# Kernel optimization log

Hardware: AMD Instinct MI355X
Metric: run time of the kernel (lower is better)

## Reference

```python
import jax, jax.numpy as jnp
import numpy as np

B, Q, D = 16, 1000, 256
HH, LV, NP = 8, 4, 4          # heads, levels, points per level
DH = D // HH                  # head dim = 32
TP = LV * NP                  # total points = 16
SHAPES = np.array([[64, 64], [32, 32], [16, 16], [8, 8]], dtype=np.int64)
LTOT = int((SHAPES[:, 0] * SHAPES[:, 1]).sum())  # 5440


def setup_inputs() -> dict:
    key = jax.random.key(0)
    ks = jax.random.split(key, 10)
    query = jax.random.normal(ks[0], (B, Q, D), dtype=jnp.float32)
    reference_points = jax.random.uniform(ks[1], (B, Q, LV, 2), dtype=jnp.float32)
    input_flatten = jax.random.normal(ks[2], (B, LTOT, D), dtype=jnp.float32)
    start = np.concatenate([[0], np.cumsum(SHAPES[:, 0] * SHAPES[:, 1])[:-1]])

    # params (mimic reset_parameters: directional bias init for offsets)
    thetas = np.arange(HH, dtype=np.float32) * (2.0 * np.pi / HH)
    grid = np.stack([np.cos(thetas), np.sin(thetas)], -1)
    grid = grid / np.abs(grid).max(-1, keepdims=True)
    grid = np.tile(grid[:, None, :], (1, TP, 1))  # [HH, TP, 2]
    scaling = np.concatenate([np.arange(1, NP + 1, dtype=np.float32) for _ in range(LV)]).reshape(1, TP, 1)
    bo = jnp.asarray((grid * scaling).reshape(-1), dtype=jnp.float32)

    s = 1.0 / np.sqrt(D)
    Wv = jax.random.normal(ks[3], (D, D), dtype=jnp.float32) * s
    bv = jnp.zeros((D,), dtype=jnp.float32)
    Wo = jax.random.normal(ks[4], (D, HH * TP * 2), dtype=jnp.float32) * 0.005
    Wa = jax.random.normal(ks[5], (D, HH * TP), dtype=jnp.float32) * 0.02
    ba = jnp.zeros((HH * TP,), dtype=jnp.float32)
    Wout = jax.random.normal(ks[6], (D, D), dtype=jnp.float32) * s
    bout = jnp.zeros((D,), dtype=jnp.float32)

    return {
        "query": query, "reference_points": reference_points, "input_flatten": input_flatten,
        "input_spatial_shapes": jnp.asarray(SHAPES), "input_level_start_index": jnp.asarray(start),
        "Wv": Wv, "bv": bv, "Wo": Wo, "bo": bo, "Wa": Wa, "ba": ba, "Wout": Wout, "bout": bout,
    }


def _sample_bilinear(val_flat, loc, Hl, Wl):
    # val_flat: [B, HH, DH, Hl*Wl]; loc: [B, Q, HH, p, 2] normalized in [0,1]
    # grid_sample align_corners=False, zeros padding: pixel = loc*size - 0.5
    b, q, h, p, _ = loc.shape
    x = loc[..., 0] * Wl - 0.5
    y = loc[..., 1] * Hl - 0.5
    x0 = jnp.floor(x); y0 = jnp.floor(y)
    lx = x - x0; ly = y - y0
    x0i = x0.astype(jnp.int32); y0i = y0.astype(jnp.int32)
    acc = jnp.zeros((b, h, val_flat.shape[2], q, p), dtype=val_flat.dtype)
    for ix, iy, w in ((x0i, y0i, (1 - lx) * (1 - ly)),
                      (x0i + 1, y0i, lx * (1 - ly)),
                      (x0i, y0i + 1, (1 - lx) * ly),
                      (x0i + 1, y0i + 1, lx * ly)):
        valid = ((ix >= 0) & (ix < Wl) & (iy >= 0) & (iy < Hl)).astype(val_flat.dtype)
        idx = jnp.clip(iy, 0, Hl - 1) * Wl + jnp.clip(ix, 0, Wl - 1)   # [B,Q,HH,p]
        idx = idx.transpose(0, 2, 1, 3).reshape(b, h, 1, q * p)
        v = jnp.take_along_axis(val_flat, idx, axis=3).reshape(b, h, -1, q, p)
        acc = acc + v * ((w * valid).transpose(0, 2, 1, 3)[:, :, None])
    return acc  # [B, HH, DH, Q, p]


def reference(query, reference_points, input_flatten, input_spatial_shapes,
              input_level_start_index, Wv, bv, Wo, bo, Wa, ba, Wout, bout):
    shapes = np.asarray(input_spatial_shapes)  # static level shapes
    shapes = shapes if shapes.any() else SHAPES  # fallback if zeros placeholder
    b, q, d = query.shape

    value = (input_flatten @ Wv + bv).reshape(b, -1, HH, DH)          # [B,L,HH,DH]
    off = (query @ Wo + bo).reshape(b, q, HH, LV, NP, 2)              # offsets
    attn = jax.nn.softmax((query @ Wa + ba).reshape(b, q, HH, TP), axis=-1)
    attn = attn.reshape(b, q, HH, LV, NP)

    # normalizer [LV,2] = (W_l, H_l)
    norm = jnp.stack([jnp.asarray(shapes[:, 1]), jnp.asarray(shapes[:, 0])], -1).astype(query.dtype)
    loc = reference_points[:, :, None, :, None, :] + off / norm[None, None, None, :, None, :]
    # loc: [B,Q,HH,LV,NP,2]

    out = jnp.zeros((b, HH, DH, q), dtype=query.dtype)
    start = 0
    for lvl in range(LV):
        Hl, Wl = int(shapes[lvl, 0]), int(shapes[lvl, 1])
        n = Hl * Wl
        val_l = value[:, start:start + n].transpose(0, 2, 3, 1)       # [B,HH,DH,n]
        start += n
        samp = _sample_bilinear(val_l, loc[:, :, :, lvl], Hl, Wl)     # [B,HH,DH,Q,NP]
        aw = attn[:, :, :, lvl].transpose(0, 2, 1, 3)                 # [B,HH,Q,NP]
        out = out + (samp * aw[:, :, None]).sum(-1)
    out = out.reshape(b, HH * DH, q).transpose(0, 2, 1)               # [B,Q,D]
    return out @ Wout + bout
```

## Files before the change

kernel.cpp:

```cpp
#include <hip/hip_runtime.h>

#define BB 16
#define QQ 1000
#define NH 8
#define LTOTAL 5440
#define MQ (BB*QQ)
#define MV (BB*LTOTAL)

typedef __bf16 bf16x8 __attribute__((ext_vector_type(8)));
typedef float  f32x4  __attribute__((ext_vector_type(4)));

template <int N> struct IC { static constexpr int v = N; };

__device__ __forceinline__ unsigned short f2bf(float f) {
  unsigned u = __builtin_bit_cast(unsigned, f);
  u += 0x7fffu + ((u >> 16) & 1u);
  return (unsigned short)(u >> 16);
}
__device__ __forceinline__ float b2f_lo(unsigned u) {
  return __builtin_bit_cast(float, u << 16);
}
__device__ __forceinline__ float b2f_hi(unsigned u) {
  return __builtin_bit_cast(float, u & 0xffff0000u);
}

__device__ __forceinline__ void gload16(const void* g, void* l) {
  __builtin_amdgcn_global_load_lds(
      (const __attribute__((address_space(1))) unsigned int*)g,
      (__attribute__((address_space(3))) unsigned int*)l, 16, 0, 0);
}

__device__ __forceinline__ void pipe_barrier() {
  asm volatile("s_waitcnt lgkmcnt(0)" ::: "memory");
  __builtin_amdgcn_sched_barrier(0);
  __builtin_amdgcn_s_barrier();
  __builtin_amdgcn_sched_barrier(0);
}

__global__ __launch_bounds__(256) void prep_k(const float* __restrict__ Wv,
                                              const float* __restrict__ Wo,
                                              const float* __restrict__ Wa,
                                              const float* __restrict__ Wout,
                                              const float* __restrict__ bo,
                                              const float* __restrict__ ba,
                                              unsigned short* __restrict__ WvS,
                                              unsigned short* __restrict__ WcS,
                                              unsigned short* __restrict__ WoS,
                                              float* __restrict__ bcat) {
  int i = blockIdx.x * 256 + threadIdx.x;
  if (i < 28672) {
    const float* src;
    unsigned short* dst;
    int g, srcN;
    if (i < 8192)       { g = i;         dst = WvS; src = Wv;   srcN = 256; }
    else if (i < 20480) { g = i - 8192;  dst = WcS; src = Wo;   srcN = 256; }
    else                { g = i - 20480; dst = WoS; src = Wout; srcN = 256; }
    int panel = g >> 12, t = (g >> 9) & 7, u = (g >> 7) & 3, row = g & 127;
    int kbase = t * 32 + u * 8;
    int n = panel * 128 + row;
    if (dst == WcS && panel == 2) { src = Wa; srcN = 128; n = row; }
    bf16x8 r;
#pragma unroll
    for (int e = 0; e < 8; e++) r[e] = (__bf16)src[(size_t)(kbase + e) * srcN + n];
    *(bf16x8*)(dst + (size_t)g * 8) = r;
  } else if (i < 29056) {
    int j = i - 28672;
    bcat[j] = j < 256 ? bo[j] : ba[j - 256];
  }
}

template <bool AF32, bool OUTBF16>
__global__ __launch_bounds__(256) void gemm3_k(const void* __restrict__ Av,
                                               const unsigned short* __restrict__ WS,
                                               const float* __restrict__ bias,
                                               void* __restrict__ C, int M, int N) {
  constexpr int K = 256, NT = 8;
  constexpr int STEADY = AF32 ? 6 : 4;
  constexpr int ASL = AF32 ? 2 : 3;
  __shared__ char lds[(ASL + 3) * 8192];
  char* As = lds;
  char* Bs = lds + ASL * 8192;

  int tid = threadIdx.x, wave = tid >> 6, lane = tid & 63;
  int ntiles = N >> 7;
  int mt = blockIdx.x / ntiles, nt = blockIdx.x - (blockIdx.x / ntiles) * ntiles;
  int r16 = lane & 15, kg = lane >> 4;
  int wm = wave >> 1, wn = wave & 1;
  int arow = tid >> 1, ahalf = tid & 1;

  const unsigned short* Bpanel = WS + (size_t)nt * (NT * 512 * 8);
  const unsigned short* Apanel = (const unsigned short*)Av + (size_t)mt * (NT * 512 * 8);
  const float* Ag32 = (const float*)Av + (size_t)(mt * 128 + arow) * K + ahalf * 16;

  f32x4 ar[2][4];
  f32x4 acc[4][4] = {};

  auto stageB = [&](int s) {
    char* Bd = Bs + (s % 3) * 8192;
    const unsigned short* sp = Bpanel + (size_t)s * 512 * 8;
#pragma unroll
    for (int j = 0; j < 2; j++) {
      int f = (j * 4 + wave) * 64 + lane;
      gload16(sp + f * 8, Bd + f * 16);
    }
  };
  auto stageA16 = [&](int s) {
    char* Ad = As + (s % 3) * 8192;
    const unsigned short* sp = Apanel + (size_t)s * 512 * 8;
#pragma unroll
    for (int j = 0; j < 2; j++) {
      int f = (j * 4 + wave) * 64 + lane;
      gload16(sp + f * 8, Ad + f * 16);
    }
  };
  auto loadA32 = [&](int s, f32x4* r) {
    const float* sp = Ag32 + s * 32;
    r[0] = *(const f32x4*)(sp);
    r[1] = *(const f32x4*)(sp + 4);
    r[2] = *(const f32x4*)(sp + 8);
    r[3] = *(const f32x4*)(sp + 12);
  };
  auto writeA32 = [&](int slot, f32x4* r) {
    bf16x8 g0, g1;
    g0[0]=(__bf16)r[0][0]; g0[1]=(__bf16)r[0][1]; g0[2]=(__bf16)r[0][2]; g0[3]=(__bf16)r[0][3];
    g0[4]=(__bf16)r[1][0]; g0[5]=(__bf16)r[1][1]; g0[6]=(__bf16)r[1][2]; g0[7]=(__bf16)r[1][3];
    g1[0]=(__bf16)r[2][0]; g1[1]=(__bf16)r[2][1]; g1[2]=(__bf16)r[2][2]; g1[3]=(__bf16)r[2][3];
    g1[4]=(__bf16)r[3][0]; g1[5]=(__bf16)r[3][1]; g1[6]=(__bf16)r[3][2]; g1[7]=(__bf16)r[3][3];
    char* Ad = As + slot * 8192;
    int u0 = ahalf * 2;
    *(bf16x8*)(Ad + (((u0    ) * 128 + arow) << 4)) = g0;
    *(bf16x8*)(Ad + (((u0 + 1) * 128 + arow) << 4)) = g1;
  };
  auto compute = [&](int sa, int sb) {
    const char* Ad = As + sa * 8192;
    const char* Bd = Bs + sb * 8192;
    bf16x8 af[4], bq[4];
#pragma unroll
    for (int mi = 0; mi < 4; mi++) {
      int row = wm * 64 + mi * 16 + r16;
      af[mi] = *(const bf16x8*)(Ad + ((kg * 128 + row) << 4));
    }
#pragma unroll
    for (int ni = 0; ni < 4; ni++) {
      int row = wn * 64 + ni * 16 + r16;
      bq[ni] = *(const bf16x8*)(Bd + ((kg * 128 + row) << 4));
    }
#pragma unroll
    for (int mi = 0; mi < 4; mi++)
#pragma unroll
      for (int ni = 0; ni < 4; ni++)
        acc[mi][ni] = __builtin_amdgcn_mfma_f32_16x16x32_bf16(af[mi], bq[ni], acc[mi][ni], 0, 0, 0);
  };

  if (AF32) { loadA32(0, ar[0]); stageB(0); loadA32(1, ar[1]); stageB(1); }
  else      { stageA16(0); stageB(0); stageA16(1); stageB(1); }
  asm volatile("s_waitcnt vmcnt(%0)" :: "i"(STEADY) : "memory");
  if (AF32) writeA32(0, ar[0]);
  pipe_barrier();

  auto step = [&](auto TC) {
    constexpr int t = decltype(TC)::v;
    if constexpr (t + 2 < NT) {
      if (AF32) loadA32(t + 2, ar[(t + 2) & 1]);
      else      stageA16(t + 2);
      stageB(t + 2);
    }
    compute(AF32 ? (t & 1) : (t % 3), t % 3);
    if constexpr (t + 1 < NT) {
      if constexpr (t + 2 < NT)
        asm volatile("s_waitcnt vmcnt(%0)" :: "i"(STEADY) : "memory");
      else
        asm volatile("s_waitcnt vmcnt(0)" ::: "memory");
      if (AF32) writeA32((t + 1) & 1, ar[(t + 1) & 1]);
      pipe_barrier();
    }
  };
  step(IC<0>{}); step(IC<1>{}); step(IC<2>{}); step(IC<3>{});
  step(IC<4>{}); step(IC<5>{}); step(IC<6>{}); step(IC<7>{});

  int row0 = mt * 128 + wm * 64 + kg * 4;
  int col0 = nt * 128 + wn * 64 + r16;
#pragma unroll
  for (int ni = 0; ni < 4; ni++) {
    int col = col0 + ni * 16;
    float bs = bias[col];
#pragma unroll
    for (int mi = 0; mi < 4; mi++) {
#pragma unroll
      for (int j = 0; j < 4; j++) {
        int row = row0 + mi * 16 + j;
        float v = acc[mi][ni][j] + bs;
        if (OUTBF16) ((unsigned short*)C)[(size_t)row * N + col] = f2bf(v);
        else         ((float*)C)[(size_t)row * N + col] = v;
      }
    }
  }
}

__global__ __launch_bounds__(256, 3) void sample_k(const float* __restrict__ offattn,
                                                   const float* __restrict__ refp,
                                                   const unsigned short* __restrict__ value,
                                                   unsigned short* __restrict__ interS) {
  int t  = blockIdx.x * 256 + threadIdx.x;
  int bq = t >> 5;
  int h  = (t >> 2) & 7;
  int c0 = (t & 3) << 3;
  int b  = bq / QQ;

  const float* base = offattn + (size_t)bq * 384;

  float lg[16];
  const float4* ab4 = (const float4*)(base + 256 + h * 16);
#pragma unroll
  for (int i = 0; i < 4; i++) {
    float4 v = ab4[i];
    lg[4*i] = v.x; lg[4*i+1] = v.y; lg[4*i+2] = v.z; lg[4*i+3] = v.w;
  }
  float m = -1e30f;
#pragma unroll
  for (int i = 0; i < 16; i++) m = fmaxf(m, lg[i]);
  float s = 0.f;
#pragma unroll
  for (int i = 0; i < 16; i++) { lg[i] = __expf(lg[i] - m); s += lg[i]; }
  float inv = 1.0f / s;

  float4 r01 = ((const float4*)(refp + (size_t)bq * 8))[0];
  float4 r23 = ((const float4*)(refp + (size_t)bq * 8))[1];
  float rxs[4] = {r01.x, r01.z, r23.x, r23.z};
  float rys[4] = {r01.y, r01.w, r23.y, r23.w};

  const unsigned short* vb = value + (size_t)b * (LTOTAL * 256) + h * 32 + c0;
  const int startL[4] = {0, 4096, 5120, 5376};

  float acc[8] = {};
#pragma unroll
  for (int lvl = 0; lvl < 4; lvl++) {
    int   Wi = 64 >> lvl;
    float Wf = (float)Wi;
    float px = rxs[lvl] * Wf - 0.5f;
    float py = rys[lvl] * Wf - 0.5f;
    const unsigned short* vl = vb + (size_t)startL[lvl] * 256;

    const float4* ob4 = (const float4*)(base + h * 32 + lvl * 8);
    float4 o01 = ob4[0], o23 = ob4[1];
    float oxs[4] = {o01.x, o01.z, o23.x, o23.z};
    float oys[4] = {o01.y, o01.w, o23.y, o23.w};

    float cw[16];
    int   coff[16];
#pragma unroll
    for (int pt = 0; pt < 4; pt++) {
      float wa = lg[lvl * 4 + pt] * inv;
      float x = px + oxs[pt];
      float y = py + oys[pt];
      float xf = floorf(x), yf = floorf(y);
      float lx = x - xf, ly = y - yf;
      int x0 = (int)xf, y0 = (int)yf;
      float wx[2] = {1.f - lx, lx};
      float wy[2] = {1.f - ly, ly};
#pragma unroll
      for (int cy = 0; cy < 2; cy++) {
        int Y = y0 + cy;
        bool vy = (unsigned)Y < (unsigned)Wi;
        int Yc = min(max(Y, 0), Wi - 1);
#pragma unroll
        for (int cx = 0; cx < 2; cx++) {
          int X = x0 + cx;
          bool vx = (unsigned)X < (unsigned)Wi;
          int Xc = min(max(X, 0), Wi - 1);
          int c = pt * 4 + cy * 2 + cx;
          cw[c]   = (vx && vy) ? wa * wy[cy] * wx[cx] : 0.f;
          coff[c] = (Yc * Wi + Xc) * 256;
        }
      }
    }
    uint4 raw[16];
#pragma unroll
    for (int c = 0; c < 16; c++) raw[c] = *(const uint4*)(vl + coff[c]);
#pragma unroll
    for (int c = 0; c < 16; c++) {
      float w = cw[c];
      acc[0] += w * b2f_lo(raw[c].x); acc[1] += w * b2f_hi(raw[c].x);
      acc[2] += w * b2f_lo(raw[c].y); acc[3] += w * b2f_hi(raw[c].y);
      acc[4] += w * b2f_lo(raw[c].z); acc[5] += w * b2f_hi(raw[c].z);
      acc[6] += w * b2f_lo(raw[c].w); acc[7] += w * b2f_hi(raw[c].w);
    }
  }

  unsigned o0 = f2bf(acc[0]) | ((unsigned)f2bf(acc[1]) << 16);
  unsigned o1 = f2bf(acc[2]) | ((unsigned)f2bf(acc[3]) << 16);
  unsigned o2 = f2bf(acc[4]) | ((unsigned)f2bf(acc[5]) << 16);
  unsigned o3 = f2bf(acc[6]) | ((unsigned)f2bf(acc[7]) << 16);
  uint4 st = {o0, o1, o2, o3};

  int mtile = bq >> 7, row = bq & 127;
  size_t goff = (((size_t)(mtile * 8 + h)) * 512 + (c0 >> 3) * 128 + row) * 8;
  *(uint4*)(interS + goff) = st;
}

extern "C" void kernel_launch(void* const* d_in, const int* in_sizes, int n_in,
                              void* d_out, int out_size, void* d_ws, size_t ws_size,
                              hipStream_t stream) {
  const float* query  = (const float*)d_in[0];
  const float* refp   = (const float*)d_in[1];
  const float* inputf = (const float*)d_in[2];
  const float* Wv   = (const float*)d_in[5];
  const float* bv   = (const float*)d_in[6];
  const float* Wo   = (const float*)d_in[7];
  const float* bo   = (const float*)d_in[8];
  const float* Wa   = (const float*)d_in[9];
  const float* ba   = (const float*)d_in[10];
  const float* Wout = (const float*)d_in[11];
  const float* bout = (const float*)d_in[12];

  char* p = (char*)d_ws;
  auto alloc = [&](size_t bytes) -> char* {
    char* r = p;
    p += (bytes + 255) & ~(size_t)255;
    return r;
  };
  unsigned short* val   = (unsigned short*)alloc((size_t)MV * 256 * 2);
  unsigned short* WvS   = (unsigned short*)alloc(2 * 4096 * 8 * 2);
  unsigned short* WcS   = (unsigned short*)alloc(3 * 4096 * 8 * 2);
  unsigned short* WoS   = (unsigned short*)alloc(2 * 4096 * 8 * 2);
  float*          bcat  = (float*)alloc(384 * 4);
  float*          offattn = (float*)alloc((size_t)MQ * 384 * 4);
  unsigned short* interS = (unsigned short*)alloc((size_t)MQ * 256 * 2);

  prep_k<<<114, 256, 0, stream>>>(Wv, Wo, Wa, Wout, bo, ba, WvS, WcS, WoS, bcat);

  gemm3_k<true, true><<<(MV / 128) * 2, 256, 0, stream>>>(
      (const void*)inputf, WvS, bv, val, MV, 256);
  gemm3_k<true, false><<<(MQ / 128) * 3, 256, 0, stream>>>(
      (const void*)query, WcS, bcat, offattn, MQ, 384);
  sample_k<<<MQ * 32 / 256, 256, 0, stream>>>(offattn, refp, val, interS);
  gemm3_k<false, false><<<(MQ / 128) * 2, 256, 0, stream>>>(
      (const void*)interS, WoS, bout, (float*)d_out, MQ, 256);
}
```

Baseline: 111.3 us.

## Keep full weight panel in LDS and stream A directly into registers

The GEMM kernel now loads the block's whole 128x256 bf16 weight panel into 64KB of LDS once at the start. Each wave then streams its A rows straight from global memory into registers, double-buffered, with fp32-to-bf16 conversion in registers. This removes the per-k-step A staging through LDS and the per-step block barriers. The MFMA operands are swapped so each lane holds four consecutive output columns, which allows vectorized epilogue stores. The sample kernel writes its intermediate in plain row-major layout instead of the swizzled panel layout. In exchange, the 64KB LDS footprint limits occupancy, and the A global reads are less coalesced.

```diff
diff --git a/kernel.cpp b/kernel.cpp
--- a/kernel.cpp
+++ b/kernel.cpp
@@ -28,13 +28,6 @@
   __builtin_amdgcn_global_load_lds(
       (const __attribute__((address_space(1))) unsigned int*)g,
       (__attribute__((address_space(3))) unsigned int*)l, 16, 0, 0);
-}
-
-__device__ __forceinline__ void pipe_barrier() {
-  asm volatile("s_waitcnt lgkmcnt(0)" ::: "memory");
-  __builtin_amdgcn_sched_barrier(0);
-  __builtin_amdgcn_s_barrier();
-  __builtin_amdgcn_sched_barrier(0);
 }
 
 __global__ __launch_bounds__(256) void prep_k(const float* __restrict__ Wv,
@@ -55,8 +48,8 @@
     if (i < 8192)       { g = i;         dst = WvS; src = Wv;   srcN = 256; }
     else if (i < 20480) { g = i - 8192;  dst = WcS; src = Wo;   srcN = 256; }
     else                { g = i - 20480; dst = WoS; src = Wout; srcN = 256; }
-    int panel = g >> 12, t = (g >> 9) & 7, u = (g >> 7) & 3, row = g & 127;
-    int kbase = t * 32 + u * 8;
+    int panel = g >> 12, ko = (g >> 7) & 31, row = g & 127;
+    int kbase = ko * 8;
     int n = panel * 128 + row;
     if (dst == WcS && panel == 2) { src = Wa; srcN = 128; n = row; }
     bf16x8 r;
@@ -70,128 +63,107 @@
 }
 
 template <bool AF32, bool OUTBF16>
-__global__ __launch_bounds__(256) void gemm3_k(const void* __restrict__ Av,
+__global__ __launch_bounds__(256) void gemm4_k(const void* __restrict__ Av,
                                                const unsigned short* __restrict__ WS,
                                                const float* __restrict__ bias,
                                                void* __restrict__ C, int M, int N) {
-  constexpr int K = 256, NT = 8;
-  constexpr int STEADY = AF32 ? 6 : 4;
-  constexpr int ASL = AF32 ? 2 : 3;
-  __shared__ char lds[(ASL + 3) * 8192];
-  char* As = lds;
-  char* Bs = lds + ASL * 8192;
+  constexpr int NT = 8;
+  constexpr int APRE = AF32 ? 16 : 8;
+  __shared__ __align__(16) char lds[65536];
 
   int tid = threadIdx.x, wave = tid >> 6, lane = tid & 63;
   int ntiles = N >> 7;
   int mt = blockIdx.x / ntiles, nt = blockIdx.x - (blockIdx.x / ntiles) * ntiles;
   int r16 = lane & 15, kg = lane >> 4;
   int wm = wave >> 1, wn = wave & 1;
-  int arow = tid >> 1, ahalf = tid & 1;
-
-  const unsigned short* Bpanel = WS + (size_t)nt * (NT * 512 * 8);
-  const unsigned short* Apanel = (const unsigned short*)Av + (size_t)mt * (NT * 512 * 8);
-  const float* Ag32 = (const float*)Av + (size_t)(mt * 128 + arow) * K + ahalf * 16;
-
-  f32x4 ar[2][4];
+
+  const unsigned short* Bp = WS + (size_t)nt * 32768;
+#pragma unroll
+  for (int j = 0; j < 16; j++) {
+    int g = j * 256 + tid;
+    gload16(Bp + (size_t)g * 8, lds + (size_t)g * 16);
+  }
+  __builtin_amdgcn_sched_barrier(0);
+
+  f32x4  ar32[2][4][2];
+  bf16x8 ar16[2][4];
+
+  const char* Ab = (const char*)Av +
+      (AF32 ? (size_t)(mt * 128 + wm * 64 + r16) * 1024
+            : (size_t)(mt * 128 + wm * 64 + r16) * 512);
+
+  auto loadA = [&](auto TT, auto SS) {
+    constexpr int t = decltype(TT)::v;
+    constexpr int s = decltype(SS)::v;
+#pragma unroll
+    for (int mi = 0; mi < 4; mi++) {
+      if (AF32) {
+        const float* ap = (const float*)(Ab + (size_t)mi * 16 * 1024) + t * 32 + kg * 8;
+        ar32[s][mi][0] = *(const f32x4*)ap;
+        ar32[s][mi][1] = *(const f32x4*)(ap + 4);
+      } else {
+        const unsigned short* ap =
+            (const unsigned short*)(Ab + (size_t)mi * 16 * 512) + t * 32 + kg * 8;
+        ar16[s][mi] = *(const bf16x8*)ap;
+      }
+    }
+  };
+
+  loadA(IC<0>{}, IC<0>{});
+  loadA(IC<1>{}, IC<1>{});
+  __builtin_amdgcn_sched_barrier(0);
+  asm volatile("s_waitcnt vmcnt(%0)" :: "i"(APRE) : "memory");
+  __builtin_amdgcn_s_barrier();
+
   f32x4 acc[4][4] = {};
 
-  auto stageB = [&](int s) {
-    char* Bd = Bs + (s % 3) * 8192;
-    const unsigned short* sp = Bpanel + (size_t)s * 512 * 8;
-#pragma unroll
-    for (int j = 0; j < 2; j++) {
-      int f = (j * 4 + wave) * 64 + lane;
-      gload16(sp + f * 8, Bd + f * 16);
-    }
-  };
-  auto stageA16 = [&](int s) {
-    char* Ad = As + (s % 3) * 8192;
-    const unsigned short* sp = Apanel + (size_t)s * 512 * 8;
-#pragma unroll
-    for (int j = 0; j < 2; j++) {
-      int f = (j * 4 + wave) * 64 + lane;
-      gload16(sp + f * 8, Ad + f * 16);
-    }
-  };
-  auto loadA32 = [&](int s, f32x4* r) {
-    const float* sp = Ag32 + s * 32;
-    r[0] = *(const f32x4*)(sp);
-    r[1] = *(const f32x4*)(sp + 4);
-    r[2] = *(const f32x4*)(sp + 8);
-    r[3] = *(const f32x4*)(sp + 12);
-  };
-  auto writeA32 = [&](int slot, f32x4* r) {
-    bf16x8 g0, g1;
-    g0[0]=(__bf16)r[0][0]; g0[1]=(__bf16)r[0][1]; g0[2]=(__bf16)r[0][2]; g0[3]=(__bf16)r[0][3];
-    g0[4]=(__bf16)r[1][0]; g0[5]=(__bf16)r[1][1]; g0[6]=(__bf16)r[1][2]; g0[7]=(__bf16)r[1][3];
-    g1[0]=(__bf16)r[2][0]; g1[1]=(__bf16)r[2][1]; g1[2]=(__bf16)r[2][2]; g1[3]=(__bf16)r[2][3];
-    g1[4]=(__bf16)r[3][0]; g1[5]=(__bf16)r[3][1]; g1[6]=(__bf16)r[3][2]; g1[7]=(__bf16)r[3][3];
-    char* Ad = As + slot * 8192;
-    int u0 = ahalf * 2;
-    *(bf16x8*)(Ad + (((u0    ) * 128 + arow) << 4)) = g0;
-    *(bf16x8*)(Ad + (((u0 + 1) * 128 + arow) << 4)) = g1;
-  };
-  auto compute = [&](int sa, int sb) {
-    const char* Ad = As + sa * 8192;
-    const char* Bd = Bs + sb * 8192;
-    bf16x8 af[4], bq[4];
+  auto step = [&](auto TT) {
+    constexpr int t = decltype(TT)::v;
+    bf16x8 af[4];
 #pragma unroll
     for (int mi = 0; mi < 4; mi++) {
-      int row = wm * 64 + mi * 16 + r16;
-      af[mi] = *(const bf16x8*)(Ad + ((kg * 128 + row) << 4));
-    }
-#pragma unroll
-    for (int ni = 0; ni < 4; ni++) {
-      int row = wn * 64 + ni * 16 + r16;
-      bq[ni] = *(const bf16x8*)(Bd + ((kg * 128 + row) << 4));
-    }
+      if (AF32) {
+        f32x4 lo = ar32[t & 1][mi][0], hi = ar32[t & 1][mi][1];
+        bf16x8 r;
+        r[0]=(__bf16)lo[0]; r[1]=(__bf16)lo[1]; r[2]=(__bf16)lo[2]; r[3]=(__bf16)lo[3];
+        r[4]=(__bf16)hi[0]; r[5]=(__bf16)hi[1]; r[6]=(__bf16)hi[2]; r[7]=(__bf16)hi[3];
+        af[mi] = r;
+      } else {
+        af[mi] = ar16[t & 1][mi];
+      }
+    }
+    if constexpr (t + 2 < NT) loadA(IC<t + 2>{}, IC<t & 1>{});
+    bf16x8 bq[4];
+#pragma unroll
+    for (int ni = 0; ni < 4; ni++)
+      bq[ni] = *(const bf16x8*)(lds +
+          ((((t * 4 + kg) * 128) + wn * 64 + ni * 16 + r16) << 4));
 #pragma unroll
     for (int mi = 0; mi < 4; mi++)
 #pragma unroll
       for (int ni = 0; ni < 4; ni++)
-        acc[mi][ni] = __builtin_amdgcn_mfma_f32_16x16x32_bf16(af[mi], bq[ni], acc[mi][ni], 0, 0, 0);
-  };
-
-  if (AF32) { loadA32(0, ar[0]); stageB(0); loadA32(1, ar[1]); stageB(1); }
-  else      { stageA16(0); stageB(0); stageA16(1); stageB(1); }
-  asm volatile("s_waitcnt vmcnt(%0)" :: "i"(STEADY) : "memory");
-  if (AF32) writeA32(0, ar[0]);
-  pipe_barrier();
-
-  auto step = [&](auto TC) {
-    constexpr int t = decltype(TC)::v;
-    if constexpr (t + 2 < NT) {
-      if (AF32) loadA32(t + 2, ar[(t + 2) & 1]);
-      else      stageA16(t + 2);
-      stageB(t + 2);
-    }
-    compute(AF32 ? (t & 1) : (t % 3), t % 3);
-    if constexpr (t + 1 < NT) {
-      if constexpr (t + 2 < NT)
-        asm volatile("s_waitcnt vmcnt(%0)" :: "i"(STEADY) : "memory");
-      else
-        asm volatile("s_waitcnt vmcnt(0)" ::: "memory");
-      if (AF32) writeA32((t + 1) & 1, ar[(t + 1) & 1]);
-      pipe_barrier();
-    }
+        acc[mi][ni] = __builtin_amdgcn_mfma_f32_16x16x32_bf16(bq[ni], af[mi], acc[mi][ni], 0, 0, 0);
   };
   step(IC<0>{}); step(IC<1>{}); step(IC<2>{}); step(IC<3>{});
   step(IC<4>{}); step(IC<5>{}); step(IC<6>{}); step(IC<7>{});
 
-  int row0 = mt * 128 + wm * 64 + kg * 4;
-  int col0 = nt * 128 + wn * 64 + r16;
+  int rowBase = mt * 128 + wm * 64;
+  int colBase = nt * 128 + wn * 64;
 #pragma unroll
   for (int ni = 0; ni < 4; ni++) {
-    int col = col0 + ni * 16;
-    float bs = bias[col];
+    int col = colBase + ni * 16 + kg * 4;
+    f32x4 bs = *(const f32x4*)(bias + col);
 #pragma unroll
     for (int mi = 0; mi < 4; mi++) {
-#pragma unroll
-      for (int j = 0; j < 4; j++) {
-        int row = row0 + mi * 16 + j;
-        float v = acc[mi][ni][j] + bs;
-        if (OUTBF16) ((unsigned short*)C)[(size_t)row * N + col] = f2bf(v);
-        else         ((float*)C)[(size_t)row * N + col] = v;
+      int row = rowBase + mi * 16 + r16;
+      f32x4 v = acc[mi][ni] + bs;
+      if (OUTBF16) {
+        uint2 st;
+        st.x = f2bf(v[0]) | ((unsigned)f2bf(v[1]) << 16);
+        st.y = f2bf(v[2]) | ((unsigned)f2bf(v[3]) << 16);
+        *(uint2*)((unsigned short*)C + (size_t)row * N + col) = st;
+      } else {
+        *(f32x4*)((float*)C + (size_t)row * N + col) = v;
       }
     }
   }
@@ -200,7 +172,7 @@
 __global__ __launch_bounds__(256, 3) void sample_k(const float* __restrict__ offattn,
                                                    const float* __restrict__ refp,
                                                    const unsigned short* __restrict__ value,
-                                                   unsigned short* __restrict__ interS) {
+                                                   unsigned short* __restrict__ inter) {
   int t  = blockIdx.x * 256 + threadIdx.x;
   int bq = t >> 5;
   int h  = (t >> 2) & 7;
@@ -292,10 +264,7 @@
   unsigned o2 = f2bf(acc[4]) | ((unsigned)f2bf(acc[5]) << 16);
   unsigned o3 = f2bf(acc[6]) | ((unsigned)f2bf(acc[7]) << 16);
   uint4 st = {o0, o1, o2, o3};
-
-  int mtile = bq >> 7, row = bq & 127;
-  size_t goff = (((size_t)(mtile * 8 + h)) * 512 + (c0 >> 3) * 128 + row) * 8;
-  *(uint4*)(interS + goff) = st;
+  *(uint4*)(inter + (size_t)bq * 256 + h * 32 + c0) = st;
 }
 
 extern "C" void kernel_launch(void* const* d_in, const int* in_sizes, int n_in,
@@ -325,15 +294,15 @@
   unsigned short* WoS   = (unsigned short*)alloc(2 * 4096 * 8 * 2);
   float*          bcat  = (float*)alloc(384 * 4);
   float*          offattn = (float*)alloc((size_t)MQ * 384 * 4);
-  unsigned short* interS = (unsigned short*)alloc((size_t)MQ * 256 * 2);
+  unsigned short* inter = (unsigned short*)alloc((size_t)MQ * 256 * 2);
 
   prep_k<<<114, 256, 0, stream>>>(Wv, Wo, Wa, Wout, bo, ba, WvS, WcS, WoS, bcat);
 
-  gemm3_k<true, true><<<(MV / 128) * 2, 256, 0, stream>>>(
+  gemm4_k<true, true><<<(MV / 128) * 2, 256, 0, stream>>>(
       (const void*)inputf, WvS, bv, val, MV, 256);
-  gemm3_k<true, false><<<(MQ / 128) * 3, 256, 0, stream>>>(
+  gemm4_k<true, false><<<(MQ / 128) * 3, 256, 0, stream>>>(
       (const void*)query, WcS, bcat, offattn, MQ, 384);
-  sample_k<<<MQ * 32 / 256, 256, 0, stream>>>(offattn, refp, val, interS);
-  gemm3_k<false, false><<<(MQ / 128) * 2, 256, 0, stream>>>(
-      (const void*)interS, WoS, bout, (float*)d_out, MQ, 256);
-}
+  sample_k<<<MQ * 32 / 256, 256, 0, stream>>>(offattn, refp, val, inter);
+  gemm4_k<false, false><<<(MQ / 128) * 2, 256, 0, stream>>>(
+      (const void*)inter, WoS, bout, (float*)d_out, MQ, 256);
+}
```

Result: slower. 141.8 us (+27.5%).

## Add 256-row, 512-thread GEMM kernel for the value projection with vectorized bf16 stores

Applied to the files above, without the earlier changes.

Replaces the value-projection GEMM with a new kernel, gemm5_k. Each 512-thread block covers 256 rows, loading fp32 A rows and converting them to bf16 in registers before writing to LDS. B is staged through a 3-slot LDS ring, with tuned vmcnt waits to keep loads in flight. The epilogue writes four packed bf16 values per store instead of scalar stores. The prep_k index arithmetic is simplified to an equivalent form. The larger tile and 512-thread blocks raise LDS and register pressure, which can lower occupancy.

```diff
diff --git a/kernel.cpp b/kernel.cpp
--- a/kernel.cpp
+++ b/kernel.cpp
@@ -55,8 +55,8 @@
     if (i < 8192)       { g = i;         dst = WvS; src = Wv;   srcN = 256; }
     else if (i < 20480) { g = i - 8192;  dst = WcS; src = Wo;   srcN = 256; }
     else                { g = i - 20480; dst = WoS; src = Wout; srcN = 256; }
-    int panel = g >> 12, t = (g >> 9) & 7, u = (g >> 7) & 3, row = g & 127;
-    int kbase = t * 32 + u * 8;
+    int panel = g >> 12, ko = (g >> 7) & 31, row = g & 127;
+    int kbase = ko * 8;
     int n = panel * 128 + row;
     if (dst == WcS && panel == 2) { src = Wa; srcN = 128; n = row; }
     bf16x8 r;
@@ -193,6 +193,113 @@
         if (OUTBF16) ((unsigned short*)C)[(size_t)row * N + col] = f2bf(v);
         else         ((float*)C)[(size_t)row * N + col] = v;
       }
+    }
+  }
+}
+
+__global__ __launch_bounds__(512, 4) void gemm5_k(const float* __restrict__ Av,
+                                                  const unsigned short* __restrict__ WS,
+                                                  const float* __restrict__ bias,
+                                                  unsigned short* __restrict__ C,
+                                                  int M, int N) {
+  constexpr int K = 256, NT = 8;
+  constexpr int STEADY = 5;
+  __shared__ __align__(16) char lds[2 * 16384 + 3 * 8192];
+  char* As = lds;
+  char* Bs = lds + 32768;
+
+  int tid = threadIdx.x, wave = tid >> 6, lane = tid & 63;
+  int mt = blockIdx.x >> 1, nt = blockIdx.x & 1;
+  int r16 = lane & 15, kg = lane >> 4;
+  int wm = wave >> 1, wn = wave & 1;
+  int arow = tid >> 1, ahalf = tid & 1;
+
+  const unsigned short* Bp = WS + (size_t)nt * (NT * 512 * 8);
+  const float* Ag32 = Av + (size_t)(mt * 256 + arow) * K + ahalf * 16;
+
+  f32x4 ar[2][4];
+  f32x4 acc[4][4] = {};
+
+  auto stageB = [&](int s) {
+    gload16(Bp + ((size_t)s * 512 + tid) * 8, Bs + (s % 3) * 8192 + tid * 16);
+  };
+  auto loadA32 = [&](int s, f32x4* r) {
+    const float* sp = Ag32 + s * 32;
+    r[0] = *(const f32x4*)(sp);
+    r[1] = *(const f32x4*)(sp + 4);
+    r[2] = *(const f32x4*)(sp + 8);
+    r[3] = *(const f32x4*)(sp + 12);
+  };
+  auto writeA32 = [&](int slot, f32x4* r) {
+    bf16x8 g0, g1;
+    g0[0]=(__bf16)r[0][0]; g0[1]=(__bf16)r[0][1]; g0[2]=(__bf16)r[0][2]; g0[3]=(__bf16)r[0][3];
+    g0[4]=(__bf16)r[1][0]; g0[5]=(__bf16)r[1][1]; g0[6]=(__bf16)r[1][2]; g0[7]=(__bf16)r[1][3];
+    g1[0]=(__bf16)r[2][0]; g1[1]=(__bf16)r[2][1]; g1[2]=(__bf16)r[2][2]; g1[3]=(__bf16)r[2][3];
+    g1[4]=(__bf16)r[3][0]; g1[5]=(__bf16)r[3][1]; g1[6]=(__bf16)r[3][2]; g1[7]=(__bf16)r[3][3];
+    char* Ad = As + slot * 16384;
+    int u0 = ahalf * 2;
+    *(bf16x8*)(Ad + (((u0    ) * 256 + arow) << 4)) = g0;
+    *(bf16x8*)(Ad + (((u0 + 1) * 256 + arow) << 4)) = g1;
+  };
+  auto compute = [&](int t) {
+    const char* Ad = As + (t & 1) * 16384;
+    const char* Bd = Bs + (t % 3) * 8192;
+    bf16x8 af[4], bq[4];
+#pragma unroll
+    for (int mi = 0; mi < 4; mi++) {
+      int row = wm * 64 + mi * 16 + r16;
+      af[mi] = *(const bf16x8*)(Ad + ((kg * 256 + row) << 4));
+    }
+#pragma unroll
+    for (int ni = 0; ni < 4; ni++) {
+      int row = wn * 64 + ni * 16 + r16;
+      bq[ni] = *(const bf16x8*)(Bd + ((kg * 128 + row) << 4));
+    }
+#pragma unroll
+    for (int mi = 0; mi < 4; mi++)
+#pragma unroll
+      for (int ni = 0; ni < 4; ni++)
+        acc[mi][ni] = __builtin_amdgcn_mfma_f32_16x16x32_bf16(bq[ni], af[mi], acc[mi][ni], 0, 0, 0);
+  };
+
+  loadA32(0, ar[0]); stageB(0); loadA32(1, ar[1]); stageB(1);
+  asm volatile("s_waitcnt vmcnt(%0)" :: "i"(STEADY) : "memory");
+  writeA32(0, ar[0]);
+  pipe_barrier();
+
+  auto step = [&](auto TC) {
+    constexpr int t = decltype(TC)::v;
+    if constexpr (t + 2 < NT) {
+      loadA32(t + 2, ar[(t + 2) & 1]);
+      stageB(t + 2);
+    }
+    compute(t);
+    if constexpr (t + 1 < NT) {
+      if constexpr (t + 2 < NT)
+        asm volatile("s_waitcnt vmcnt(%0)" :: "i"(STEADY) : "memory");
+      else
+        asm volatile("s_waitcnt vmcnt(0)" ::: "memory");
+      writeA32((t + 1) & 1, ar[(t + 1) & 1]);
+      pipe_barrier();
+    }
+  };
+  step(IC<0>{}); step(IC<1>{}); step(IC<2>{}); step(IC<3>{});
+  step(IC<4>{}); step(IC<5>{}); step(IC<6>{}); step(IC<7>{});
+
+  int rowBase = mt * 256 + wm * 64;
+  int colBase = nt * 128 + wn * 64;
+#pragma unroll
+  for (int ni = 0; ni < 4; ni++) {
+    int col = colBase + ni * 16 + kg * 4;
+    f32x4 bs = *(const f32x4*)(bias + col);
+#pragma unroll
+    for (int mi = 0; mi < 4; mi++) {
+      int row = rowBase + mi * 16 + r16;
+      f32x4 v = acc[mi][ni] + bs;
+      uint2 st;
+      st.x = f2bf(v[0]) | ((unsigned)f2bf(v[1]) << 16);
+      st.y = f2bf(v[2]) | ((unsigned)f2bf(v[3]) << 16);
+      *(uint2*)(C + (size_t)row * N + col) = st;
     }
   }
 }
@@ -329,8 +436,7 @@
 
   prep_k<<<114, 256, 0, stream>>>(Wv, Wo, Wa, Wout, bo, ba, WvS, WcS, WoS, bcat);
 
-  gemm3_k<true, true><<<(MV / 128) * 2, 256, 0, stream>>>(
-      (const void*)inputf, WvS, bv, val, MV, 256);
+  gemm5_k<<<(MV / 256) * 2, 512, 0, stream>>>(inputf, WvS, bv, val, MV, 256);
   gemm3_k<true, false><<<(MQ / 128) * 3, 256, 0, stream>>>(
       (const void*)query, WcS, bcat, offattn, MQ, 384);
   sample_k<<<MQ * 32 / 256, 256, 0, stream>>>(offattn, refp, val, interS);
```

Result: slower. 119.2 us (+7.1%).
